# Optimization experiments

Measured on AMD Instinct MI355X. Metric: run time of the kernel, lower is better.

The kernel has to match this reference:

```python
import jax, jax.numpy as jnp
import numpy as np

B, T, C = 2, 2048, 2048
NH, NKV, D = 16, 4, 128
N_REP = NH // NKV
THETA = 10000.0


def setup_inputs() -> dict:
    key = jax.random.key(0)
    ks = jax.random.split(key, 5)
    s = 0.02
    return {
        "x": jax.random.normal(ks[0], (B, T, C), dtype=jnp.float32),
        "Wq": jax.random.normal(ks[1], (C, C), dtype=jnp.float32) * s,
        "Wk": jax.random.normal(ks[2], (NKV * D, C), dtype=jnp.float32) * s,
        "Wv": jax.random.normal(ks[3], (NKV * D, C), dtype=jnp.float32) * s,
        "Wo": jax.random.normal(ks[4], (C, C), dtype=jnp.float32) * s,
    }


def _rope(t):
    # t: (B, H, T, D); rotate pairs (even, odd) by angle pos * theta_i
    inv_freq = 1.0 / (THETA ** (jnp.arange(0, D, 2, dtype=jnp.float32) / D))  # (D/2,)
    ang = jnp.arange(T, dtype=jnp.float32)[:, None] * inv_freq[None, :]       # (T, D/2)
    cos, sin = jnp.cos(ang), jnp.sin(ang)
    te, to = t[..., 0::2], t[..., 1::2]
    re = te * cos - to * sin
    ro = te * sin + to * cos
    return jnp.stack([re, ro], axis=-1).reshape(t.shape).astype(t.dtype)


def reference(x, Wq, Wk, Wv, Wo):
    # Projections (Linear: y = x @ W.T)
    q = (x @ Wq.T).reshape(B, T, NH, D).transpose(0, 2, 1, 3)    # (B,NH,T,D)
    k = (x @ Wk.T).reshape(B, T, NKV, D).transpose(0, 2, 1, 3)   # (B,NKV,T,D)
    v = (x @ Wv.T).reshape(B, T, NKV, D).transpose(0, 2, 1, 3)
    q = _rope(q)
    k = _rope(k)
    # GQA: group query heads per kv head instead of materializing repeated K/V
    qg = q.reshape(B, NKV, N_REP, T, D)                          # (B,G,R,T,D)
    scale = 1.0 / jnp.sqrt(jnp.float32(D))
    scores = jnp.einsum("bgrtd,bgsd->bgrts", qg, k) * scale      # (B,G,R,T,T)
    causal = jnp.tril(jnp.ones((T, T), dtype=bool))
    scores = jnp.where(causal, scores, jnp.finfo(scores.dtype).min)
    attn = jax.nn.softmax(scores, axis=-1)
    out = jnp.einsum("bgrts,bgsd->bgrtd", attn, v)               # (B,G,R,T,D)
    out = out.reshape(B, NH, T, D).transpose(0, 2, 1, 3).reshape(B, T, C)
    return out @ Wo.T
```

## Files before the change

### kernel.cpp

```cpp
#include <hip/hip_runtime.h>
#include <hip/hip_bf16.h>
#include <stdint.h>

#define B_   2
#define T_   2048
#define C_   2048
#define NH_  16
#define NKV_ 4
#define D_   128
#define NREP_ 4

typedef __attribute__((ext_vector_type(8))) short bf16x8;
typedef __attribute__((ext_vector_type(4))) float f32x4;

__device__ inline short f2bs(float f) {
    __hip_bfloat16 h = __float2bfloat16(f);
    return *reinterpret_cast<short*>(&h);
}

__device__ inline void gl_lds16(const __hip_bfloat16* g, __hip_bfloat16* l) {
    __builtin_amdgcn_global_load_lds(
        (const __attribute__((address_space(1))) unsigned int*)g,
        (__attribute__((address_space(3))) unsigned int*)l,
        16, 0, 0);
}

__global__ void prep_kernel(const float* __restrict__ x,  const float* __restrict__ Wq,
                            const float* __restrict__ Wk, const float* __restrict__ Wv,
                            const float* __restrict__ Wo,
                            __hip_bfloat16* __restrict__ xb, __hip_bfloat16* __restrict__ wcat,
                            __hip_bfloat16* __restrict__ wob, float2* __restrict__ ropeTab) {
    int tid = blockIdx.x * blockDim.x + threadIdx.x;
    const int CVT_THREADS = 4718592;
    if (tid < CVT_THREADS) {
        int i4 = tid * 4;
        const float* src;
        __hip_bfloat16* dst;
        int off;
        if (i4 < 8388608)       { src = x;  dst = xb;             off = i4; }
        else if (i4 < 12582912) { src = Wq; dst = wcat;           off = i4 - 8388608; }
        else if (i4 < 13631488) { src = Wk; dst = wcat + 4194304; off = i4 - 12582912; }
        else if (i4 < 14680064) { src = Wv; dst = wcat + 5242880; off = i4 - 13631488; }
        else                    { src = Wo; dst = wob;            off = i4 - 14680064; }
        float4 v = *reinterpret_cast<const float4*>(src + off);
        short4 o;
        o.x = f2bs(v.x); o.y = f2bs(v.y); o.z = f2bs(v.z); o.w = f2bs(v.w);
        *reinterpret_cast<short4*>(dst + off) = o;
    } else {
        int e = tid - CVT_THREADS;
        if (e < 131072) {
            int t = e >> 6, p = e & 63;
            float inv = __expf(-(float)p * (9.210340371976184f / 64.0f));
            float ang = (float)t * inv;
            ropeTab[e] = make_float2(cosf(ang), sinf(ang));
        }
    }
}

template <int MODE, int BN, int NTN>
__global__ __launch_bounds__(512, 2) void gemm_ff(
    const __hip_bfloat16* __restrict__ A,
    const __hip_bfloat16* __restrict__ Bm,
    const float2* __restrict__ ropeTab,
    __hip_bfloat16* __restrict__ qo,
    __hip_bfloat16* __restrict__ ko,
    __hip_bfloat16* __restrict__ vT,
    float* __restrict__ Cout) {
    constexpr int K = 2048;
    constexpr int NT = K / 64;
    constexpr int WN = BN / 64;
    constexpr int WM = 8 / WN;
    constexpr int RPW = 256 / WM;
    constexpr int MI_T = RPW / 16;
    constexpr int BSZ = BN * 64;
    constexpr int BLOADS = BSZ / 8192;
    extern __shared__ char lds[];

    const int tid = threadIdx.x;
    const int lane = tid & 63;
    const int wid = tid >> 6;
    const int wm = wid / WN, wn = wid % WN;
    const int q16 = lane >> 4, r16 = lane & 15;

    const int cpx = (int)gridDim.x >> 3;
    const int bs = ((int)blockIdx.x & 7) * cpx + ((int)blockIdx.x >> 3);
    const int tm = bs / NTN, tn = bs % NTN;
    const int rmA = tm * 256, rmB = tn * BN;

    const int csw = (q16 << 4) ^ ((r16 & 3) << 4);

    f32x4 acc[MI_T][4] = {};
    bf16x8 aF[MI_T], bF[4];

#define STG_A(buf_, sl_, kstep_)                                                     \
    { _Pragma("unroll") for (int li = 0; li < 2; li++) {                             \
        const int L_ = li * 8192 + tid * 16;                                         \
        const int rw_ = L_ >> 6;                                                     \
        const int cb_ = (L_ & 63) ^ ((rw_ & 3) << 4);                                \
        gl_lds16(A + (size_t)(rmA + rw_) * K + (kstep_) * 64 + (sl_) * 32 + (cb_ >> 1), \
                 (__hip_bfloat16*)(lds + (buf_) * 32768 + (sl_) * 16384 + L_));      \
    } }
#define STG_B(buf_, sl_, kstep_)                                                     \
    { _Pragma("unroll") for (int li = 0; li < BLOADS; li++) {                        \
        const int L_ = li * 8192 + tid * 16;                                         \
        const int rw_ = L_ >> 6;                                                     \
        const int cb_ = (L_ & 63) ^ ((rw_ & 3) << 4);                                \
        gl_lds16(Bm + (size_t)(rmB + rw_) * K + (kstep_) * 64 + (sl_) * 32 + (cb_ >> 1), \
                 (__hip_bfloat16*)(lds + 65536 + (buf_) * 2 * BSZ + (sl_) * BSZ + L_)); \
    } }
#define RD_A(buf_, sl_)                                                              \
    { _Pragma("unroll") for (int mi = 0; mi < MI_T; mi++)                            \
        aF[mi] = *(const bf16x8*)(lds + (buf_) * 32768 + (sl_) * 16384 +             \
                                  (wm * RPW + mi * 16 + r16) * 64 + csw); }
#define RD_B(buf_, sl_)                                                              \
    { _Pragma("unroll") for (int bi = 0; bi < 4; bi++)                               \
        bF[bi] = *(const bf16x8*)(lds + 65536 + (buf_) * 2 * BSZ + (sl_) * BSZ +     \
                                  (wn * 64 + bi * 16 + r16) * 64 + csw); }
#define MM_                                                                          \
    { __builtin_amdgcn_s_setprio(1);                                                 \
      _Pragma("unroll") for (int mi = 0; mi < MI_T; mi++)                            \
      _Pragma("unroll") for (int bi = 0; bi < 4; bi++)                               \
          acc[mi][bi] = __builtin_amdgcn_mfma_f32_16x16x32_bf16(                     \
              aF[mi], bF[bi], acc[mi][bi], 0, 0, 0);                                 \
      __builtin_amdgcn_s_setprio(0); }
#define VMC                                                                          \
    { if constexpr (BLOADS == 2) { asm volatile("s_waitcnt vmcnt(4)" ::: "memory"); } \
      else                       { asm volatile("s_waitcnt vmcnt(3)" ::: "memory"); } }
#define BAR __builtin_amdgcn_s_barrier()

    STG_A(0, 0, 0); STG_B(0, 0, 0);
    STG_A(0, 1, 0); STG_B(0, 1, 0);
    VMC; BAR;

    for (int u = 0; u < NT - 1; u++) {
        const int bf_ = u & 1;
        RD_A(bf_, 0); RD_B(bf_, 0);
        STG_A(bf_ ^ 1, 0, u + 1); STG_B(bf_ ^ 1, 0, u + 1);
        MM_;
        VMC; BAR;
        RD_A(bf_, 1); RD_B(bf_, 1);
        STG_A(bf_ ^ 1, 1, u + 1); STG_B(bf_ ^ 1, 1, u + 1);
        MM_;
        VMC; BAR;
    }
    {
        const int bf_ = (NT - 1) & 1;
        RD_A(bf_, 0); RD_B(bf_, 0);
        MM_;
        asm volatile("s_waitcnt vmcnt(0)" ::: "memory"); BAR;
        RD_A(bf_, 1); RD_B(bf_, 1);
        MM_;
    }
#undef BAR
#undef VMC
#undef MM_
#undef RD_B
#undef RD_A
#undef STG_B
#undef STG_A

    if constexpr (MODE == 0) {
        constexpr int N = NTN * BN;
        float* const cbase = Cout + (size_t)(rmA + wm * RPW) * N + tn * BN + wn * 64 + r16;
#pragma unroll
        for (int mi = 0; mi < MI_T; mi++)
#pragma unroll
            for (int r = 0; r < 4; r++) {
                float* dst = cbase + (size_t)(mi * 16 + q16 * 4 + r) * N;
#pragma unroll
                for (int bi = 0; bi < 4; bi++)
                    dst[bi * 16] = acc[mi][bi][r];
            }
    } else {
        const int hb = tn * 2 + (wn >> 1);
        const float sgn = (r16 & 1) ? 1.0f : -1.0f;
#pragma unroll
        for (int mi = 0; mi < MI_T; mi++)
#pragma unroll
            for (int r = 0; r < 4; r++) {
                const int m = rmA + wm * RPW + mi * 16 + q16 * 4 + r;
                const int bb = m >> 11, t = m & 2047;
                if (hb < 20) {
                    const float2* tabRow = ropeTab + t * 64;
                    __hip_bfloat16* dst = (hb < 16)
                        ? qo + ((size_t)(bb * NH_ + hb) * T_ + t) * D_
                        : ko + ((size_t)(bb * NKV_ + (hb - 16)) * T_ + t) * D_;
#pragma unroll
                    for (int bi = 0; bi < 4; bi++) {
                        const int dloc = (wn & 1) * 64 + bi * 16 + r16;
                        float v = acc[mi][bi][r];
                        float prt = __shfl_xor(v, 1);
                        float2 cs = tabRow[dloc >> 1];
                        dst[dloc] = __float2bfloat16(fmaf(prt * sgn, cs.y, v * cs.x));
                    }
                } else {
                    __hip_bfloat16* dst = vT + (size_t)(bb * NKV_ + (hb - 20)) * D_ * T_ + t;
#pragma unroll
                    for (int bi = 0; bi < 4; bi++) {
                        const int dloc = (wn & 1) * 64 + bi * 16 + r16;
                        dst[(size_t)dloc * T_] = __float2bfloat16(acc[mi][bi][r]);
                    }
                }
            }
    }
}

__global__ __launch_bounds__(256, 3) void attn_kernel(const __hip_bfloat16* __restrict__ Q,
                                                      const __hip_bfloat16* __restrict__ Kt,
                                                      const __hip_bfloat16* __restrict__ Vt,
                                                      __hip_bfloat16* __restrict__ Ao,
                                                      float* __restrict__ O0,
                                                      float* __restrict__ O1,
                                                      float* __restrict__ l0p,
                                                      float* __restrict__ l1p) {
    __shared__ __hip_bfloat16 Ks[2][4096];
    __shared__ __hip_bfloat16 Vs[2][4096];
    __shared__ __hip_bfloat16 Pl[4][1280];

    const int lane = threadIdx.x & 63, wv = threadIdx.x >> 6;
    const int bg = blockIdx.y;
    const int u  = (int)blockIdx.x;
    int tb, nIt, sIdx;
    if (u < 32)      { tb = u;      nIt = tb + 1;      sIdx = -1; }
    else if (u < 64) { tb = u;      nIt = 32;          sIdx = 0;  }
    else             { tb = u - 32; nIt = tb + 1 - 32; sIdx = 1;  }
    const int sBase = (sIdx == 1) ? 1024 : 0;
    const int b = bg >> 2, g = bg & 3;
    const int h = g * 4 + wv;
    const int t0 = tb * 32;
    const int q16 = lane >> 4, r16 = lane & 15;

    const __hip_bfloat16* qh = Q + ((size_t)((b * NH_ + h) * T_) + t0) * D_;
    const __hip_bfloat16* kh = Kt + (size_t)(b * NKV_ + g) * T_ * D_;
    const __hip_bfloat16* vh = Vt + (size_t)(b * NKV_ + g) * D_ * T_;

    bf16x8 bqA[4], bqB[4];
#pragma unroll
    for (int kk = 0; kk < 4; kk++) {
        bqA[kk] = *reinterpret_cast<const bf16x8*>(qh + (size_t)r16 * D_ + kk * 32 + q16 * 8);
        bqB[kk] = *reinterpret_cast<const bf16x8*>(qh + (size_t)(16 + r16) * D_ + kk * 32 + q16 * 8);
    }

    float liA = 0.f, liB = 0.f;
    f32x4 oA[8], oB[8];
#pragma unroll
    for (int d = 0; d < 8; d++) {
        oA[d] = (f32x4){0.f, 0.f, 0.f, 0.f};
        oB[d] = (f32x4){0.f, 0.f, 0.f, 0.f};
    }

    const float SCL2 = 0.088388347648318447f * 1.4426950408889634f;
    const int tqA = t0 + r16;
    const int tqB = t0 + 16 + r16;

    const __hip_bfloat16* gK = kh + (size_t)((wv & 1) * 16 + r16) * D_ + q16 * 8;
    const __hip_bfloat16* gV = vh + (size_t)(((wv - 2) * 4) * 16 + r16) * T_ + q16 * 8;

#define STAGE(bufi, s0_)                                                        \
    do {                                                                        \
        if (wv < 2) {                                                           \
            const __hip_bfloat16* gp = gK + (size_t)(s0_) * D_;                 \
            __hip_bfloat16* lp = &Ks[bufi][(wv * 4) * 512] + lane * 8;          \
            gl_lds16(gp,      lp);                                              \
            gl_lds16(gp + 32, lp + 512);                                        \
            gl_lds16(gp + 64, lp + 1024);                                      \
            gl_lds16(gp + 96, lp + 1536);                                      \
        } else {                                                                \
            const __hip_bfloat16* gp = gV + (s0_);                              \
            __hip_bfloat16* lp = &Vs[bufi][((wv - 2) * 4) * 512] + lane * 8;    \
            gl_lds16(gp,                      lp);                              \
            gl_lds16(gp + (size_t)16 * T_,    lp + 512);                        \
            gl_lds16(gp + (size_t)32 * T_,    lp + 1024);                      \
            gl_lds16(gp + (size_t)48 * T_,    lp + 1536);                      \
        }                                                                       \
    } while (0)

    STAGE(0, sBase);

    for (int j = 0; j < nIt; j++) {
        const int s0 = sBase + j * 32;
        const int cur = j & 1;
        __syncthreads();
        if (j + 1 < nIt) STAGE(cur ^ 1, s0 + 32);

        f32x4 sc0A = (f32x4){0.f, 0.f, 0.f, 0.f};
        f32x4 sc1A = (f32x4){0.f, 0.f, 0.f, 0.f};
        f32x4 sc0B = (f32x4){0.f, 0.f, 0.f, 0.f};
        f32x4 sc1B = (f32x4){0.f, 0.f, 0.f, 0.f};
        {
            bf16x8 ak[4];
#pragma unroll
            for (int kk = 0; kk < 4; kk++)
                ak[kk] = *reinterpret_cast<const bf16x8*>(&Ks[cur][kk * 512] + lane * 8);
#pragma unroll
            for (int kk = 0; kk < 4; kk++) {
                sc0A = __builtin_amdgcn_mfma_f32_16x16x32_bf16(ak[kk], bqA[kk], sc0A, 0, 0, 0);
                sc0B = __builtin_amdgcn_mfma_f32_16x16x32_bf16(ak[kk], bqB[kk], sc0B, 0, 0, 0);
            }
#pragma unroll
            for (int kk = 0; kk < 4; kk++)
                ak[kk] = *reinterpret_cast<const bf16x8*>(&Ks[cur][(4 + kk) * 512] + lane * 8);
#pragma unroll
            for (int kk = 0; kk < 4; kk++) {
                sc1A = __builtin_amdgcn_mfma_f32_16x16x32_bf16(ak[kk], bqA[kk], sc1A, 0, 0, 0);
                sc1B = __builtin_amdgcn_mfma_f32_16x16x32_bf16(ak[kk], bqB[kk], sc1B, 0, 0, 0);
            }
        }

        ushort4 w0A, w1A, w0B, w1B;
        float psA = 0.f, psB = 0.f;
        if (s0 + 32 > t0) {
#pragma unroll
            for (int r = 0; r < 4; r++) {
                int s_a = s0 + q16 * 4 + r;
                float pa0 = (s_a <= tqA)      ? __builtin_amdgcn_exp2f(sc0A[r] * SCL2) : 0.f;
                float pa1 = (s_a + 16 <= tqA) ? __builtin_amdgcn_exp2f(sc1A[r] * SCL2) : 0.f;
                float pb0 = (s_a <= tqB)      ? __builtin_amdgcn_exp2f(sc0B[r] * SCL2) : 0.f;
                float pb1 = (s_a + 16 <= tqB) ? __builtin_amdgcn_exp2f(sc1B[r] * SCL2) : 0.f;
                psA += pa0 + pa1;
                psB += pb0 + pb1;
                ((unsigned short*)&w0A)[r] = (unsigned short)f2bs(pa0);
                ((unsigned short*)&w1A)[r] = (unsigned short)f2bs(pa1);
                ((unsigned short*)&w0B)[r] = (unsigned short)f2bs(pb0);
                ((unsigned short*)&w1B)[r] = (unsigned short)f2bs(pb1);
            }
        } else {
#pragma unroll
            for (int r = 0; r < 4; r++) {
                float pa0 = __builtin_amdgcn_exp2f(sc0A[r] * SCL2);
                float pa1 = __builtin_amdgcn_exp2f(sc1A[r] * SCL2);
                float pb0 = __builtin_amdgcn_exp2f(sc0B[r] * SCL2);
                float pb1 = __builtin_amdgcn_exp2f(sc1B[r] * SCL2);
                psA += pa0 + pa1;
                psB += pb0 + pb1;
                ((unsigned short*)&w0A)[r] = (unsigned short)f2bs(pa0);
                ((unsigned short*)&w1A)[r] = (unsigned short)f2bs(pa1);
                ((unsigned short*)&w0B)[r] = (unsigned short)f2bs(pb0);
                ((unsigned short*)&w1B)[r] = (unsigned short)f2bs(pb1);
            }
        }
        liA += psA;
        liB += psB;

        *reinterpret_cast<ushort4*>(&Pl[wv][r16 * 40 + q16 * 4]) = w0A;
        *reinterpret_cast<ushort4*>(&Pl[wv][r16 * 40 + 16 + q16 * 4]) = w1A;
        *reinterpret_cast<ushort4*>(&Pl[wv][640 + r16 * 40 + q16 * 4]) = w0B;
        *reinterpret_cast<ushort4*>(&Pl[wv][640 + r16 * 40 + 16 + q16 * 4]) = w1B;
        asm volatile("s_waitcnt lgkmcnt(0)" ::: "memory");
        bf16x8 pfA = *reinterpret_cast<const bf16x8*>(&Pl[wv][r16 * 40 + q16 * 8]);
        bf16x8 pfB = *reinterpret_cast<const bf16x8*>(&Pl[wv][640 + r16 * 40 + q16 * 8]);

#pragma unroll
        for (int d = 0; d < 8; d++) {
            bf16x8 bv = *reinterpret_cast<const bf16x8*>(&Vs[cur][d * 512] + lane * 8);
            oA[d] = __builtin_amdgcn_mfma_f32_16x16x32_bf16(pfA, bv, oA[d], 0, 0, 0);
            oB[d] = __builtin_amdgcn_mfma_f32_16x16x32_bf16(pfB, bv, oB[d], 0, 0, 0);
        }
    }

    liA += __shfl_xor(liA, 16);
    liA += __shfl_xor(liA, 32);
    liB += __shfl_xor(liB, 16);
    liB += __shfl_xor(liB, 32);

    if (sIdx < 0) {
#pragma unroll
        for (int r = 0; r < 4; r++) {
            float lrA = __shfl(liA, q16 * 4 + r, 16);
            float lrB = __shfl(liB, q16 * 4 + r, 16);
            float invA = 1.0f / lrA;
            float invB = 1.0f / lrB;
            int tA = t0 + q16 * 4 + r;
            __hip_bfloat16* dstA = Ao + (size_t)(b * T_ + tA) * C_ + h * D_ + r16;
            __hip_bfloat16* dstB = dstA + (size_t)16 * C_;
#pragma unroll
            for (int d = 0; d < 8; d++) {
                dstA[d * 16] = __float2bfloat16(oA[d][r] * invA);
                dstB[d * 16] = __float2bfloat16(oB[d][r] * invB);
            }
        }
    } else {
        float* Os = (sIdx == 0) ? O0 : O1;
        float* ls = (sIdx == 0) ? l0p : l1p;
        const size_t rb = (size_t)(b * NH_ + h) * 1024 + (size_t)(t0 - 1024);
        if (q16 == 0) {
            ls[rb + r16]      = liA;
            ls[rb + 16 + r16] = liB;
        }
#pragma unroll
        for (int r = 0; r < 4; r++) {
            int rowl = q16 * 4 + r;
            float* dA = Os + (rb + rowl) * 128 + r16;
            float* dB = Os + (rb + 16 + rowl) * 128 + r16;
#pragma unroll
            for (int d = 0; d < 8; d++) {
                dA[d * 16] = oA[d][r];
                dB[d * 16] = oB[d][r];
            }
        }
    }
#undef STAGE
}

__global__ void attn_combine(const float* __restrict__ O0, const float* __restrict__ O1,
                             const float* __restrict__ l0, const float* __restrict__ l1,
                             __hip_bfloat16* __restrict__ Ao) {
    int idx = blockIdx.x * blockDim.x + threadIdx.x;
    int row = idx >> 5, d4 = (idx & 31) << 2;
    int bh = row >> 10, tl = row & 1023;
    int b = bh >> 4, h = bh & 15;
    float inv = 1.0f / (l0[row] + l1[row]);
    float4 a = *reinterpret_cast<const float4*>(O0 + (size_t)row * 128 + d4);
    float4 c = *reinterpret_cast<const float4*>(O1 + (size_t)row * 128 + d4);
    short4 o;
    o.x = f2bs((a.x + c.x) * inv);
    o.y = f2bs((a.y + c.y) * inv);
    o.z = f2bs((a.z + c.z) * inv);
    o.w = f2bs((a.w + c.w) * inv);
    *reinterpret_cast<short4*>(Ao + (size_t)(b * T_ + 1024 + tl) * C_ + h * D_ + d4) = o;
}

extern "C" void kernel_launch(void* const* d_in, const int* in_sizes, int n_in,
                              void* d_out, int out_size, void* d_ws, size_t ws_size,
                              hipStream_t stream) {
    const float* x  = (const float*)d_in[0];
    const float* Wq = (const float*)d_in[1];
    const float* Wk = (const float*)d_in[2];
    const float* Wv = (const float*)d_in[3];
    const float* Wo = (const float*)d_in[4];
    float* out = (float*)d_out;
    char* ws = (char*)d_ws;

    __hip_bfloat16* xb   = (__hip_bfloat16*)(ws + 0);
    __hip_bfloat16* wcat = (__hip_bfloat16*)(ws + 16777216);
    float2*         ropeTab = (float2*)(ws + 29360128);
    __hip_bfloat16* wob  = (__hip_bfloat16*)(ws + 30408704);
    __hip_bfloat16* qatt = (__hip_bfloat16*)(ws + 38797312);
    __hip_bfloat16* katt = (__hip_bfloat16*)(ws + 55574528);
    __hip_bfloat16* vT   = (__hip_bfloat16*)(ws + 59768832);
    __hip_bfloat16* aout = (__hip_bfloat16*)(ws + 63963136);
    float* O0 = (float*)(ws + 0);
    float* O1 = (float*)(ws + 80740352);
    float* l0 = (float*)(ws + 97517568);
    float* l1 = (float*)(ws + 97648640);

    static bool s_attr_done = false;
    if (!s_attr_done) {
        hipFuncSetAttribute(reinterpret_cast<const void*>(&gemm_ff<1, 256, 12>),
                            hipFuncAttributeMaxDynamicSharedMemorySize, 131072);
        hipFuncSetAttribute(reinterpret_cast<const void*>(&gemm_ff<0, 128, 16>),
                            hipFuncAttributeMaxDynamicSharedMemorySize, 98304);
        s_attr_done = true;
    }

    const int thr = 256;
    prep_kernel<<<18944, thr, 0, stream>>>(x, Wq, Wk, Wv, Wo, xb, wcat, wob, ropeTab);

    gemm_ff<1, 256, 12><<<192, 512, 131072, stream>>>(xb, wcat, ropeTab, qatt, katt, vT, nullptr);

    attn_kernel<<<dim3(96, 8), 256, 0, stream>>>(qatt, katt, vT, aout, O0, O1, l0, l1);
    attn_combine<<<(2 * NH_ * 1024 * 32) / thr, thr, 0, stream>>>(O0, O1, l0, l1, aout);

    gemm_ff<0, 128, 16><<<256, 512, 98304, stream>>>(aout, wob, nullptr, nullptr, nullptr, nullptr, out);
}
```

Measured before the change: 293.0 us.

## Replace QKV projection GEMM with simpler 128x128-tile kernel

Swaps the tuned multi-stage gemm_ff QKV path (256-wide tiles, 512 threads, 128KB dynamic LDS) for a new gemm_qkv kernel. The new kernel uses 128x128 tiles with a K-step of 32, 256 threads, static LDS, and a synchronous load-then-compute loop with no double buffering. RoPE is applied in the epilogue via a lane shuffle, and V is written transposed. This trades pipelining and larger-tile reuse for a simpler kernel with more blocks, which risks exposed load latency and uncoalesced transposed stores.

New measurement: 282.9 us. 1.04x faster.

```diff
diff --git a/kernel.cpp b/kernel.cpp
--- a/kernel.cpp
+++ b/kernel.cpp
@@ -55,6 +55,85 @@
             ropeTab[e] = make_float2(cosf(ang), sinf(ang));
         }
     }
+}
+
+__global__ __launch_bounds__(256) void gemm_qkv(const __hip_bfloat16* __restrict__ A,
+                                                const __hip_bfloat16* __restrict__ Bm,
+                                                const float2* __restrict__ ropeTab,
+                                                __hip_bfloat16* __restrict__ qo,
+                                                __hip_bfloat16* __restrict__ ko,
+                                                __hip_bfloat16* __restrict__ vT) {
+    const int K = 2048;
+    __shared__ __hip_bfloat16 As[128 * 32];
+    __shared__ __hip_bfloat16 Bs[128 * 32];
+    const int tid  = threadIdx.x;
+    const int lane = tid & 63;
+    const int wv   = tid >> 6;
+    const int m0 = blockIdx.y * 128, n0 = blockIdx.x * 128;
+    const int wm = (wv >> 1) * 64, wn = (wv & 1) * 64;
+    const int q16 = lane >> 4, r16 = lane & 15;
+
+    f32x4 acc[4][4] = {};
+
+    const int lrow = tid >> 2;
+    const int lcol = (tid & 3) * 8;
+    const __hip_bfloat16* aG = A  + (size_t)(m0 + lrow) * K + lcol;
+    const __hip_bfloat16* bG = Bm + (size_t)(n0 + lrow) * K + lcol;
+    __hip_bfloat16* aL = As + tid * 8;
+    __hip_bfloat16* bL = Bs + tid * 8;
+
+    for (int k0 = 0; k0 < K; k0 += 32) {
+        __syncthreads();
+        gl_lds16(aG + k0,          aL);
+        gl_lds16(aG + 64 * K + k0, aL + 2048);
+        gl_lds16(bG + k0,          bL);
+        gl_lds16(bG + 64 * K + k0, bL + 2048);
+        __syncthreads();
+        bf16x8 af[4], bfr[4];
+#pragma unroll
+        for (int i = 0; i < 4; i++)
+            af[i] = *reinterpret_cast<const bf16x8*>(As + (wm + i * 16 + r16) * 32 + q16 * 8);
+#pragma unroll
+        for (int j = 0; j < 4; j++)
+            bfr[j] = *reinterpret_cast<const bf16x8*>(Bs + (wn + j * 16 + r16) * 32 + q16 * 8);
+#pragma unroll
+        for (int i = 0; i < 4; i++)
+#pragma unroll
+            for (int j = 0; j < 4; j++)
+                acc[i][j] = __builtin_amdgcn_mfma_f32_16x16x32_bf16(af[i], bfr[j], acc[i][j], 0, 0, 0);
+    }
+
+    const int hb = n0 >> 7;
+    const float sgn = (r16 & 1) ? 1.0f : -1.0f;
+#pragma unroll
+    for (int i = 0; i < 4; i++)
+#pragma unroll
+        for (int r = 0; r < 4; r++) {
+            const int m = m0 + wm + i * 16 + q16 * 4 + r;
+            const int b = m >> 11, t = m & 2047;
+            if (hb < 20) {
+                const float2* tabRow = ropeTab + t * 64;
+                __hip_bfloat16* dst = (hb < 16)
+                    ? qo + ((size_t)(b * NH_ + hb) * T_ + t) * D_
+                    : ko + ((size_t)(b * NKV_ + (hb - 16)) * T_ + t) * D_;
+#pragma unroll
+                for (int j = 0; j < 4; j++) {
+                    const int dloc = wn + j * 16 + r16;
+                    float v = acc[i][j][r];
+                    float prt = __shfl_xor(v, 1);
+                    float2 cs = tabRow[dloc >> 1];
+                    float res = fmaf(prt * sgn, cs.y, v * cs.x);
+                    dst[dloc] = __float2bfloat16(res);
+                }
+            } else {
+                __hip_bfloat16* dst = vT + (size_t)(b * NKV_ + (hb - 20)) * D_ * T_ + t;
+#pragma unroll
+                for (int j = 0; j < 4; j++) {
+                    const int d = wn + j * 16 + r16;
+                    dst[(size_t)d * T_] = __float2bfloat16(acc[i][j][r]);
+                }
+            }
+        }
 }
 
 template <int MODE, int BN, int NTN>
@@ -446,8 +525,6 @@
 
     static bool s_attr_done = false;
     if (!s_attr_done) {
-        hipFuncSetAttribute(reinterpret_cast<const void*>(&gemm_ff<1, 256, 12>),
-                            hipFuncAttributeMaxDynamicSharedMemorySize, 131072);
         hipFuncSetAttribute(reinterpret_cast<const void*>(&gemm_ff<0, 128, 16>),
                             hipFuncAttributeMaxDynamicSharedMemorySize, 98304);
         s_attr_done = true;
@@ -456,7 +533,7 @@
     const int thr = 256;
     prep_kernel<<<18944, thr, 0, stream>>>(x, Wq, Wk, Wv, Wo, xb, wcat, wob, ropeTab);
 
-    gemm_ff<1, 256, 12><<<192, 512, 131072, stream>>>(xb, wcat, ropeTab, qatt, katt, vT, nullptr);
+    gemm_qkv<<<dim3(24, 32), 256, 0, stream>>>(xb, wcat, ropeTab, qatt, katt, vT);
 
     attn_kernel<<<dim3(96, 8), 256, 0, stream>>>(qatt, katt, vT, aout, O0, O1, l0, l1);
     attn_combine<<<(2 * NH_ * 1024 * 32) / thr, thr, 0, stream>>>(O0, O1, l0, l1, aout);
```
